# Performance work log

Measured on AMD Instinct MI355X. Metric: run time of the kernel, lower is better.

## Reference

```python
import jax, jax.numpy as jnp
import numpy as np
from jax import lax

BS, L, HID = 16, 512, 768
H, HD, NREG = 12, 64, 8
R2 = 2 * NREG


def setup_inputs() -> dict:
    key = jax.random.key(0)
    ks = jax.random.split(key, 7)
    s = 1.0 / np.sqrt(HID)
    return {
        "hidden_states": jax.random.normal(ks[0], (BS, L, HID), jnp.float32),
        "K1_w": jax.random.normal(ks[1], (H * HD, HID), jnp.float32) * s,
        "K1_b": jnp.zeros((H * HD,), jnp.float32),
        "V1_w": jax.random.normal(ks[2], (H * HD, HID), jnp.float32) * s,
        "V1_b": jnp.zeros((H * HD,), jnp.float32),
        "reading_head": jax.random.normal(ks[3], (H, HD), jnp.float32) * (1.0 / np.sqrt(HD)),
        "bidirection_weight": jnp.ones((1, 1, H, 1, R2), jnp.float32) * (1.0 / R2),
    }


def _softmax_dim1(x):
    # torch: softmax over length dim (1) plus 1/exp(max) residual term
    m = jnp.max(x, axis=1, keepdims=True)
    e = jnp.exp(x - m)
    return e / jnp.sum(e, axis=1, keepdims=True) + jnp.exp(-m)


def _cummax_idx(e):
    # torch.cummax indices over axis=1 for a bool tensor (ties -> latest index):
    # last True index so far; if no True yet, current index.
    ar = jnp.arange(e.shape[1], dtype=jnp.int32)[None, :, None]
    lt = lax.cummax(jnp.where(e, ar, jnp.int32(-1)), axis=1)
    return jnp.where(lt >= 0, lt, ar)


def reference(hidden_states, K1_w, K1_b, V1_w, V1_b, reading_head, bidirection_weight):
    bs, length, _ = hidden_states.shape
    K1 = jax.nn.relu(hidden_states @ K1_w.T + K1_b).reshape(bs, length, H, HD)
    V1 = jax.nn.relu(hidden_states @ V1_w.T + V1_b).reshape(bs, length, H, HD)

    scores = jnp.einsum("blhn,hn->blh", K1, reading_head)
    events = _softmax_dim1(scores) > (1.5 / length)  # (bs, L, H) bool; fwd==bwd for IC1

    col0 = _cummax_idx(events)  # (bs, L, H)
    rolled = jnp.roll(events, -1, axis=1)
    col1 = jnp.flip(512 - _cummax_idx(jnp.flip(rolled, axis=1)), axis=1)
    col1 = col1.at[:, 0].set(0)

    # sequential shift-register scan over length
    e_seq = jnp.moveaxis(events, 1, 0)  # (L, bs, H)
    f_seq = jnp.moveaxis(col0, 1, 0)
    b_seq = jnp.moveaxis(col1, 1, 0)
    row0 = jnp.concatenate(
        [f_seq[0][:, None], b_seq[0][:, None], jnp.zeros((bs, R2, H), jnp.int32)], axis=1
    )  # (bs, R2+2, H)

    def step(row, inp):
        e, f, b = inp
        reg = jnp.where(e[:, None, :], row[:, :-2], row[:, 2:])  # shift-in on event
        new_row = jnp.concatenate([f[:, None], b[:, None], reg], axis=1)
        return new_row, reg

    _, regs = lax.scan(step, row0, (e_seq[1:], f_seq[1:], b_seq[1:]))
    regs = jnp.concatenate([jnp.zeros((1, bs, R2, H), jnp.int32), regs], axis=0)  # (L,bs,R2,H)
    idx = jnp.moveaxis(regs, 0, 1).reshape(bs, length * R2, H)
    idx = jnp.clip(idx, 0, length - 1)

    V2 = jnp.take_along_axis(V1, idx[..., None], axis=1).reshape(bs, length, R2, H, HD)
    w = bidirection_weight.reshape(H, R2)
    return jnp.einsum("blrhd,hr->blhd", V2, w)  # (bs, L, H, HD)
```

## Files before the change

kernel.cpp:

```cpp
#include <hip/hip_runtime.h>
#include <cstdint>
#include <cstddef>

#define BSZ 16
#define LQ  512
#define HIDDIM 768
#define NH  12
#define HD  64
#define R2V 16
#define NTOT 1536
#define MTOT 8192

typedef __bf16 bf16x8 __attribute__((ext_vector_type(8)));
typedef float  f32x4  __attribute__((ext_vector_type(4)));

__device__ inline unsigned short f2bf(float x) {
    union { float f; unsigned u; } c; c.f = x;
    unsigned r = c.u + 0x7fffu + ((c.u >> 16) & 1u);
    return (unsigned short)(r >> 16);
}
__device__ inline float bfl(unsigned u) { return __uint_as_float(u << 16); }
__device__ inline float bfh(unsigned u) { return __uint_as_float(u & 0xffff0000u); }

__device__ inline unsigned pk2bf(float x, float y) {
#if __has_builtin(__builtin_amdgcn_cvt_pk_bf16_f32)
    typedef __bf16 bf16x2 __attribute__((ext_vector_type(2)));
    union { bf16x2 v; unsigned u; } c;
    c.v = __builtin_amdgcn_cvt_pk_bf16_f32(x, y);
    return c.u;
#else
    return (unsigned)f2bf(x) | ((unsigned)f2bf(y) << 16);
#endif
}

#define TBM 128
#define TBN 128
#define TBK 32
#define KITERS (HIDDIM / TBK)

__global__ __launch_bounds__(256, 3) void gemm_fused(
    const float* __restrict__ hs,
    const float* __restrict__ Kw, const float* __restrict__ Vw,
    const float* __restrict__ Kb, const float* __restrict__ Vb,
    unsigned short* __restrict__ K1b, unsigned short* __restrict__ V1b)
{
    __shared__ unsigned short As[2][TBM * TBK];
    __shared__ unsigned short Bs[2][TBN * TBK];

    const int n0   = blockIdx.x * TBN;
    const int m0   = blockIdx.y * TBM;
    const int tid  = threadIdx.x;
    const int wid  = tid >> 6;
    const int lane = tid & 63;
    const int wm   = (wid & 1) * 64;
    const int wn   = (wid >> 1) * 64;

    const bool isK = (n0 < HIDDIM);
    const float* __restrict__ Wsrc = isK ? Kw : Vw;
    const float* __restrict__ bias = isK ? Kb : Vb;
    const int ncol0 = isK ? n0 : (n0 - HIDDIM);

    f32x4 acc[4][4] = {};

    const int r0 = wid * 32;
    const int rA = r0 + (lane >> 1);
    const int kh = (lane & 1) * 16;

    const float* Aptr = hs   + (size_t)(m0 + rA) * HIDDIM + kh;
    const float* Bptr = Wsrc + (size_t)(ncol0 + rA) * HIDDIM + kh;

    uint4* AsD = (uint4*)&As[0][rA * TBK + kh];
    uint4* BsD = (uint4*)&Bs[0][rA * TBK + kh];
    const int bufStride16 = (TBM * TBK) / 8;

    float4 ar0, ar1, ar2, ar3, br0, br1, br2, br3;

#define LOADREGS(kof)                                     \
    do {                                                  \
        ar0 = *(const float4*)(Aptr + (kof));             \
        ar1 = *(const float4*)(Aptr + (kof) + 4);         \
        ar2 = *(const float4*)(Aptr + (kof) + 8);         \
        ar3 = *(const float4*)(Aptr + (kof) + 12);        \
        br0 = *(const float4*)(Bptr + (kof));             \
        br1 = *(const float4*)(Bptr + (kof) + 4);         \
        br2 = *(const float4*)(Bptr + (kof) + 8);         \
        br3 = *(const float4*)(Bptr + (kof) + 12);        \
    } while (0)

#define CVTSTORE(buf)                                                         \
    do {                                                                      \
        uint4 p;                                                              \
        p.x = pk2bf(ar0.x, ar0.y); p.y = pk2bf(ar0.z, ar0.w);                 \
        p.z = pk2bf(ar1.x, ar1.y); p.w = pk2bf(ar1.z, ar1.w);                 \
        AsD[(buf) * bufStride16] = p;                                         \
        p.x = pk2bf(ar2.x, ar2.y); p.y = pk2bf(ar2.z, ar2.w);                 \
        p.z = pk2bf(ar3.x, ar3.y); p.w = pk2bf(ar3.z, ar3.w);                 \
        AsD[(buf) * bufStride16 + 1] = p;                                     \
        p.x = pk2bf(br0.x, br0.y); p.y = pk2bf(br0.z, br0.w);                 \
        p.z = pk2bf(br1.x, br1.y); p.w = pk2bf(br1.z, br1.w);                 \
        BsD[(buf) * bufStride16] = p;                                         \
        p.x = pk2bf(br2.x, br2.y); p.y = pk2bf(br2.z, br2.w);                 \
        p.z = pk2bf(br3.x, br3.y); p.w = pk2bf(br3.z, br3.w);                 \
        BsD[(buf) * bufStride16 + 1] = p;                                     \
    } while (0)

    const int fm = lane & 15;
    const int fk = (lane >> 4) * 8;

    LOADREGS(0);
    CVTSTORE(0);

    for (int it = 0; it < KITERS; ++it) {
        __syncthreads();
        const int cb = it & 1;
        if (it + 1 < KITERS) LOADREGS((it + 1) * TBK);

        bf16x8 af[4], bfr[4];
        #pragma unroll
        for (int mi = 0; mi < 4; ++mi)
            af[mi] = *reinterpret_cast<const bf16x8*>(&As[cb][(wm + mi * 16 + fm) * TBK + fk]);
        #pragma unroll
        for (int ni = 0; ni < 4; ++ni)
            bfr[ni] = *reinterpret_cast<const bf16x8*>(&Bs[cb][(wn + ni * 16 + fm) * TBK + fk]);
        #pragma unroll
        for (int mi = 0; mi < 4; ++mi)
            #pragma unroll
            for (int ni = 0; ni < 4; ++ni)
                acc[mi][ni] = __builtin_amdgcn_mfma_f32_16x16x32_bf16(
                    bfr[ni], af[mi], acc[mi][ni], 0, 0, 0);

        if (it + 1 < KITERS) CVTSTORE(cb ^ 1);
    }
#undef LOADREGS
#undef CVTSTORE

    unsigned short* __restrict__ dst = isK ? K1b : V1b;
    const int mloc = lane & 15;
    const int nq   = (lane >> 4) * 4;

    #pragma unroll
    for (int mi = 0; mi < 4; ++mi) {
        const int mg = m0 + wm + mi * 16 + mloc;
        #pragma unroll
        for (int ni = 0; ni < 4; ++ni) {
            const int col = ncol0 + wn + ni * 16 + nq;
            float4 bv = *(const float4*)(bias + col);
            f32x4 a = acc[mi][ni];
            ushort4 o;
            o.x = f2bf(fmaxf(a[0] + bv.x, 0.f));
            o.y = f2bf(fmaxf(a[1] + bv.y, 0.f));
            o.z = f2bf(fmaxf(a[2] + bv.z, 0.f));
            o.w = f2bf(fmaxf(a[3] + bv.w, 0.f));
            *(ushort4*)(dst + (size_t)mg * HIDDIM + col) = o;
        }
    }
}

#define SINF (1 << 30)
#define IXP 17

__global__ __launch_bounds__(512) void scan_gather(
    const unsigned short* __restrict__ K1b,
    const unsigned short* __restrict__ V1b,
    const float* __restrict__ rh,
    const float* __restrict__ bw,
    float* __restrict__ out)
{
    const int bh   = blockIdx.x;
    const int b    = bh / NH;
    const int h    = bh % NH;
    const int l    = threadIdx.x;
    const int lane = l & 63;
    const int wid  = l >> 6;

    __shared__ float wredA[8];
    __shared__ float wredB[8];
    __shared__ int   wp0[8];
    __shared__ int   wp1[8];
    __shared__ int   wp2[8];
    __shared__ int   ev[LQ];
    __shared__ int   col0[LQ];
    __shared__ int   col1[LQ];
    __shared__ int   E[LQ];
    __shared__ int   idxs[LQ * IXP];
    __shared__ float wsm[R2V];

    if (l < R2V) wsm[l] = bw[h * R2V + l];

    const unsigned short* krow = K1b + ((size_t)(b * LQ + l)) * HIDDIM + h * HD;
    const float* rrow = rh + h * HD;
    float s = 0.f;
    #pragma unroll
    for (int c8 = 0; c8 < 8; ++c8) {
        uint4 kv = *(const uint4*)(krow + c8 * 8);
        float4 ra = *(const float4*)(rrow + c8 * 8);
        float4 rb = *(const float4*)(rrow + c8 * 8 + 4);
        s += bfl(kv.x) * ra.x + bfh(kv.x) * ra.y
           + bfl(kv.y) * ra.z + bfh(kv.y) * ra.w
           + bfl(kv.z) * rb.x + bfh(kv.z) * rb.y
           + bfl(kv.w) * rb.z + bfh(kv.w) * rb.w;
    }

    float mx = s;
    #pragma unroll
    for (int off = 32; off > 0; off >>= 1) mx = fmaxf(mx, __shfl_xor(mx, off));
    if (lane == 0) wredA[wid] = mx;
    __syncthreads();
    float m = wredA[0];
    #pragma unroll
    for (int i = 1; i < 8; ++i) m = fmaxf(m, wredA[i]);

    const float e = expf(s - m);
    float sm = e;
    #pragma unroll
    for (int off = 32; off > 0; off >>= 1) sm += __shfl_xor(sm, off);
    if (lane == 0) wredB[wid] = sm;
    __syncthreads();
    float ssum = 0.f;
    #pragma unroll
    for (int i = 0; i < 8; ++i) ssum += wredB[i];

    const float p = e / ssum + expf(-m);
    const int event = (p > (1.5f / 512.0f)) ? 1 : 0;
    ev[l] = event;

    int v = event ? l : -1;
    #pragma unroll
    for (int off = 1; off < 64; off <<= 1) {
        int u = __shfl_up(v, off);
        if (lane >= off) v = (u > v) ? u : v;
    }
    if (lane == 63) wp0[wid] = v;
    __syncthreads();
    int pfx = -1;
    for (int i = 0; i < wid; ++i) pfx = (wp0[i] > pfx) ? wp0[i] : pfx;
    v = (pfx > v) ? pfx : v;
    col0[l] = (v >= 0) ? v : l;

    int v1 = ev[(l + 1) & (LQ - 1)] ? l : SINF;
    #pragma unroll
    for (int off = 1; off < 64; off <<= 1) {
        int u = __shfl_down(v1, off);
        if (lane < 64 - off) v1 = (u < v1) ? u : v1;
    }
    if (lane == 0) wp1[wid] = v1;
    __syncthreads();
    int sfx = SINF;
    for (int i = wid + 1; i < 8; ++i) sfx = (wp1[i] < sfx) ? wp1[i] : sfx;
    v1 = (sfx < v1) ? sfx : v1;
    col1[l] = (l == 0) ? 0 : (((v1 < SINF) ? v1 : l) + 1);

    int c = (l >= 1) ? event : 0;
    #pragma unroll
    for (int off = 1; off < 64; off <<= 1) {
        int u = __shfl_up(c, off);
        if (lane >= off) c += u;
    }
    if (lane == 63) wp2[wid] = c;
    __syncthreads();
    for (int i = 0; i < wid; ++i) c += wp2[i];

    if (l >= 1 && event) E[c - 1] = l;
    __syncthreads();

    int* op = &idxs[l * IXP];
    #pragma unroll
    for (int j = 0; j < 8; ++j) {
        const int k = c - 1 - j;
        int f = 0, bb = 0;
        if (k >= 0) {
            const int t = E[k];
            f  = col0[t - 1];
            bb = col1[t - 1];
        }
        op[2 * j]     = min(max(f, 0), LQ - 1);
        op[2 * j + 1] = min(max(bb, 0), LQ - 1);
    }
    __syncthreads();

    const int dsl = lane & 7;
    const size_t vbase = (size_t)b * LQ * HIDDIM + h * HD + dsl * 8;

    for (int round = 0; round < 8; ++round) {
        const int lg = round * 64 + wid * 8 + (lane >> 3);
        const int* ip = &idxs[lg * IXP];
        float a0 = 0.f, a1 = 0.f, a2 = 0.f, a3 = 0.f;
        float a4 = 0.f, a5 = 0.f, a6 = 0.f, a7 = 0.f;
        #pragma unroll 1
        for (int rc = 0; rc < R2V; rc += 4) {
            const int i0 = ip[rc], i1 = ip[rc + 1], i2 = ip[rc + 2], i3 = ip[rc + 3];
            uint4 v0 = *(const uint4*)(V1b + vbase + (size_t)i0 * HIDDIM);
            uint4 vA = *(const uint4*)(V1b + vbase + (size_t)i1 * HIDDIM);
            uint4 vB = *(const uint4*)(V1b + vbase + (size_t)i2 * HIDDIM);
            uint4 vC = *(const uint4*)(V1b + vbase + (size_t)i3 * HIDDIM);
            const float w0 = wsm[rc], w1 = wsm[rc + 1], w2 = wsm[rc + 2], w3 = wsm[rc + 3];
            a0 += w0 * bfl(v0.x); a1 += w0 * bfh(v0.x);
            a2 += w0 * bfl(v0.y); a3 += w0 * bfh(v0.y);
            a4 += w0 * bfl(v0.z); a5 += w0 * bfh(v0.z);
            a6 += w0 * bfl(v0.w); a7 += w0 * bfh(v0.w);
            a0 += w1 * bfl(vA.x); a1 += w1 * bfh(vA.x);
            a2 += w1 * bfl(vA.y); a3 += w1 * bfh(vA.y);
            a4 += w1 * bfl(vA.z); a5 += w1 * bfh(vA.z);
            a6 += w1 * bfl(vA.w); a7 += w1 * bfh(vA.w);
            a0 += w2 * bfl(vB.x); a1 += w2 * bfh(vB.x);
            a2 += w2 * bfl(vB.y); a3 += w2 * bfh(vB.y);
            a4 += w2 * bfl(vB.z); a5 += w2 * bfh(vB.z);
            a6 += w2 * bfl(vB.w); a7 += w2 * bfh(vB.w);
            a0 += w3 * bfl(vC.x); a1 += w3 * bfh(vC.x);
            a2 += w3 * bfl(vC.y); a3 += w3 * bfh(vC.y);
            a4 += w3 * bfl(vC.z); a5 += w3 * bfh(vC.z);
            a6 += w3 * bfl(vC.w); a7 += w3 * bfh(vC.w);
        }
        float* po = out + ((size_t)(b * LQ + lg) * NH + h) * HD + dsl * 8;
        *(float4*)po       = make_float4(a0, a1, a2, a3);
        *((float4*)po + 1) = make_float4(a4, a5, a6, a7);
    }
}

extern "C" void kernel_launch(void* const* d_in, const int* in_sizes, int n_in,
                              void* d_out, int out_size, void* d_ws, size_t ws_size,
                              hipStream_t stream)
{
    (void)in_sizes; (void)n_in; (void)out_size; (void)ws_size;

    const float* hs = (const float*)d_in[0];
    const float* Kw = (const float*)d_in[1];
    const float* Kb = (const float*)d_in[2];
    const float* Vw = (const float*)d_in[3];
    const float* Vb = (const float*)d_in[4];
    const float* rh = (const float*)d_in[5];
    const float* bw = (const float*)d_in[6];
    float* out = (float*)d_out;

    char* ws = (char*)d_ws;
    unsigned short* K1b = (unsigned short*)(ws);
    unsigned short* V1b = (unsigned short*)(ws + 12582912);

    dim3 g1(NTOT / TBN, MTOT / TBM);
    gemm_fused<<<g1, 256, 0, stream>>>(hs, Kw, Vw, Kb, Vb, K1b, V1b);

    scan_gather<<<BSZ * NH, LQ, 0, stream>>>(K1b, V1b, rh, bw, out);
}
```

Before: 161.4 us.

## Pre-cast weights to bf16 and stage GEMM tiles via direct global-to-LDS loads

Adds a small kernel that converts the K and V projection weights to bf16 in workspace once per call. The GEMM then stages the fp32 activation tile and the bf16 weight tile straight into LDS using global_load_lds with XOR-swizzled layouts, and converts activations to bf16 at fragment-read time. The aim is to remove the register round-trip and the convert-then-store step from the load pipeline and to halve weight bandwidth. In exchange it adds a kernel launch, doubles LDS for the A tile by keeping it in fp32, and drops the occupancy hint on launch bounds.

```diff
diff --git a/kernel.cpp b/kernel.cpp
--- a/kernel.cpp
+++ b/kernel.cpp
@@ -33,19 +33,46 @@
 #endif
 }
 
+#define NW1 147456
+#define NW4 294912
+
+__global__ __launch_bounds__(256) void cast_w(
+    const float* __restrict__ Kw, const float* __restrict__ Vw,
+    unsigned short* __restrict__ Wbf)
+{
+    const int i = blockIdx.x * 256 + threadIdx.x;
+    float4 v = (i < NW1) ? ((const float4*)Kw)[i] : ((const float4*)Vw)[i - NW1];
+    ushort4 o;
+    o.x = f2bf(v.x); o.y = f2bf(v.y); o.z = f2bf(v.z); o.w = f2bf(v.w);
+    *(ushort4*)(Wbf + (size_t)i * 4) = o;
+}
+
 #define TBM 128
 #define TBN 128
 #define TBK 32
 #define KITERS (HIDDIM / TBK)
 
-__global__ __launch_bounds__(256, 3) void gemm_fused(
+#define GLD16(g, l) __builtin_amdgcn_global_load_lds( \
+    (const __attribute__((address_space(1))) void*)(g), \
+    (__attribute__((address_space(3))) void*)(l), 16, 0, 0)
+
+__device__ inline bf16x8 ldAfrag(const float* p) {
+    float4 x = *(const float4*)p;
+    float4 y = *(const float4*)(p + 4);
+    union { uint4 u; bf16x8 v; } c;
+    c.u.x = pk2bf(x.x, x.y); c.u.y = pk2bf(x.z, x.w);
+    c.u.z = pk2bf(y.x, y.y); c.u.w = pk2bf(y.z, y.w);
+    return c.v;
+}
+
+__global__ __launch_bounds__(256) void gemm_hyb(
     const float* __restrict__ hs,
-    const float* __restrict__ Kw, const float* __restrict__ Vw,
+    const unsigned short* __restrict__ Wbf,
     const float* __restrict__ Kb, const float* __restrict__ Vb,
     unsigned short* __restrict__ K1b, unsigned short* __restrict__ V1b)
 {
-    __shared__ unsigned short As[2][TBM * TBK];
-    __shared__ unsigned short Bs[2][TBN * TBK];
+    __shared__ float          Asf[2][TBM * TBK];
+    __shared__ unsigned short Bsb[2][TBN * TBK];
 
     const int n0   = blockIdx.x * TBN;
     const int m0   = blockIdx.y * TBM;
@@ -56,83 +83,56 @@
     const int wn   = (wid >> 1) * 64;
 
     const bool isK = (n0 < HIDDIM);
-    const float* __restrict__ Wsrc = isK ? Kw : Vw;
     const float* __restrict__ bias = isK ? Kb : Vb;
     const int ncol0 = isK ? n0 : (n0 - HIDDIM);
 
     f32x4 acc[4][4] = {};
 
     const int r0 = wid * 32;
-    const int rA = r0 + (lane >> 1);
-    const int kh = (lane & 1) * 16;
-
-    const float* Aptr = hs   + (size_t)(m0 + rA) * HIDDIM + kh;
-    const float* Bptr = Wsrc + (size_t)(ncol0 + rA) * HIDDIM + kh;
-
-    uint4* AsD = (uint4*)&As[0][rA * TBK + kh];
-    uint4* BsD = (uint4*)&Bs[0][rA * TBK + kh];
-    const int bufStride16 = (TBM * TBK) / 8;
-
-    float4 ar0, ar1, ar2, ar3, br0, br1, br2, br3;
-
-#define LOADREGS(kof)                                     \
-    do {                                                  \
-        ar0 = *(const float4*)(Aptr + (kof));             \
-        ar1 = *(const float4*)(Aptr + (kof) + 4);         \
-        ar2 = *(const float4*)(Aptr + (kof) + 8);         \
-        ar3 = *(const float4*)(Aptr + (kof) + 12);        \
-        br0 = *(const float4*)(Bptr + (kof));             \
-        br1 = *(const float4*)(Bptr + (kof) + 4);         \
-        br2 = *(const float4*)(Bptr + (kof) + 8);         \
-        br3 = *(const float4*)(Bptr + (kof) + 12);        \
-    } while (0)
-
-#define CVTSTORE(buf)                                                         \
-    do {                                                                      \
-        uint4 p;                                                              \
-        p.x = pk2bf(ar0.x, ar0.y); p.y = pk2bf(ar0.z, ar0.w);                 \
-        p.z = pk2bf(ar1.x, ar1.y); p.w = pk2bf(ar1.z, ar1.w);                 \
-        AsD[(buf) * bufStride16] = p;                                         \
-        p.x = pk2bf(ar2.x, ar2.y); p.y = pk2bf(ar2.z, ar2.w);                 \
-        p.z = pk2bf(ar3.x, ar3.y); p.w = pk2bf(ar3.z, ar3.w);                 \
-        AsD[(buf) * bufStride16 + 1] = p;                                     \
-        p.x = pk2bf(br0.x, br0.y); p.y = pk2bf(br0.z, br0.w);                 \
-        p.z = pk2bf(br1.x, br1.y); p.w = pk2bf(br1.z, br1.w);                 \
-        BsD[(buf) * bufStride16] = p;                                         \
-        p.x = pk2bf(br2.x, br2.y); p.y = pk2bf(br2.z, br2.w);                 \
-        p.z = pk2bf(br3.x, br3.y); p.w = pk2bf(br3.z, br3.w);                 \
-        BsD[(buf) * bufStride16 + 1] = p;                                     \
+    const int aRow   = r0 + (lane >> 3);
+    const int aChunk = (lane & 7) ^ ((lane >> 3) & 6);
+    const float* ApG = hs + (size_t)(m0 + aRow) * HIDDIM + aChunk * 4;
+    const int bRow   = r0 + (lane >> 2);
+    const int bChunk = (lane & 3) ^ ((lane >> 3) & 3);
+    const unsigned short* BpG = Wbf + (size_t)(n0 + bRow) * HIDDIM + bChunk * 8;
+
+#define STAGE(buf, kof)                                              \
+    do {                                                             \
+        GLD16(ApG + (kof),               &Asf[buf][(r0     ) * TBK]);\
+        GLD16(ApG + (kof) +  8 * HIDDIM, &Asf[buf][(r0 +  8) * TBK]);\
+        GLD16(ApG + (kof) + 16 * HIDDIM, &Asf[buf][(r0 + 16) * TBK]);\
+        GLD16(ApG + (kof) + 24 * HIDDIM, &Asf[buf][(r0 + 24) * TBK]);\
+        GLD16(BpG + (kof),               &Bsb[buf][(r0     ) * TBK]);\
+        GLD16(BpG + (kof) + 16 * HIDDIM, &Bsb[buf][(r0 + 16) * TBK]);\
     } while (0)
 
     const int fm = lane & 15;
     const int fk = (lane >> 4) * 8;
-
-    LOADREGS(0);
-    CVTSTORE(0);
+    const int aOff = (((fk >> 2) ^ (fm & 6)) << 2);
+    const int bOff = (((fk >> 3) ^ ((fm >> 1) & 3)) << 3);
+
+    STAGE(0, 0);
 
     for (int it = 0; it < KITERS; ++it) {
         __syncthreads();
         const int cb = it & 1;
-        if (it + 1 < KITERS) LOADREGS((it + 1) * TBK);
+        if (it + 1 < KITERS) STAGE(cb ^ 1, (it + 1) * TBK);
 
         bf16x8 af[4], bfr[4];
         #pragma unroll
         for (int mi = 0; mi < 4; ++mi)
-            af[mi] = *reinterpret_cast<const bf16x8*>(&As[cb][(wm + mi * 16 + fm) * TBK + fk]);
+            af[mi] = ldAfrag(&Asf[cb][(wm + mi * 16 + fm) * TBK + aOff]);
         #pragma unroll
         for (int ni = 0; ni < 4; ++ni)
-            bfr[ni] = *reinterpret_cast<const bf16x8*>(&Bs[cb][(wn + ni * 16 + fm) * TBK + fk]);
+            bfr[ni] = *reinterpret_cast<const bf16x8*>(&Bsb[cb][(wn + ni * 16 + fm) * TBK + bOff]);
         #pragma unroll
         for (int mi = 0; mi < 4; ++mi)
             #pragma unroll
             for (int ni = 0; ni < 4; ++ni)
                 acc[mi][ni] = __builtin_amdgcn_mfma_f32_16x16x32_bf16(
                     bfr[ni], af[mi], acc[mi][ni], 0, 0, 0);
-
-        if (it + 1 < KITERS) CVTSTORE(cb ^ 1);
-    }
-#undef LOADREGS
-#undef CVTSTORE
+    }
+#undef STAGE
 
     unsigned short* __restrict__ dst = isK ? K1b : V1b;
     const int mloc = lane & 15;
@@ -335,9 +335,12 @@
     char* ws = (char*)d_ws;
     unsigned short* K1b = (unsigned short*)(ws);
     unsigned short* V1b = (unsigned short*)(ws + 12582912);
+    unsigned short* Wbf = (unsigned short*)(ws + 25165824);
+
+    cast_w<<<NW4 / 256, 256, 0, stream>>>(Kw, Vw, Wbf);
 
     dim3 g1(NTOT / TBN, MTOT / TBM);
-    gemm_fused<<<g1, 256, 0, stream>>>(hs, Kw, Vw, Kb, Vb, K1b, V1b);
+    gemm_hyb<<<g1, 256, 0, stream>>>(hs, Wbf, Kb, Vb, K1b, V1b);
 
     scan_gather<<<BSZ * NH, LQ, 0, stream>>>(K1b, V1b, rh, bw, out);
 }
```

Result: slower. 179.5 us (+11.2%).
